# Kernel optimization log

Measured on AMD Instinct MI355X. Metric: run time of the kernel, lower is better.

## Reference

```python
import jax, jax.numpy as jnp
import numpy as np
from jax import lax


def _maxpool_nchw(x, k):
    # Non-overlapping kxk max pool over the last two dims (NCHW).
    return lax.reduce_window(x, -jnp.inf, lax.max,
                             window_dimensions=(1, 1, k, k),
                             window_strides=(1, 1, k, k),
                             padding='VALID')


def setup_inputs() -> dict:
    key = jax.random.key(0)
    k1, k2, k3, k4, k5 = jax.random.split(key, 5)
    B = 16
    return {
        'input_tensor1': jax.random.normal(k1, (B, 128, 48, 48), jnp.float32),
        'input_tensor2': jax.random.normal(k2, (B, 64, 96, 96), jnp.float32),
        'input_tensor3': jax.random.normal(k3, (B, 32, 192, 192), jnp.float32),
        'input_tensor4': jax.random.normal(k4, (B, 16, 384, 384), jnp.float32),
        'pure_ff': jax.random.normal(k5, (B, 256, 24, 24), jnp.float32),
    }


def reference(input_tensor1, input_tensor2, input_tensor3, input_tensor4, pure_ff):
    # and then max-pools. Pooling is per-channel, so this equals pooling once
    # and tiling the pooled result along the channel axis -- same math,
    # without materializing the redundant concat intermediates.
    x1 = jnp.tile(_maxpool_nchw(input_tensor1, 2), (1, 2, 1, 1))   # [B,256,24,24]
    x2 = jnp.tile(_maxpool_nchw(input_tensor2, 4), (1, 4, 1, 1))   # [B,256,24,24]
    x3 = jnp.tile(_maxpool_nchw(input_tensor3, 8), (1, 8, 1, 1))   # [B,256,24,24]
    x4 = jnp.tile(_maxpool_nchw(input_tensor4, 16), (1, 16, 1, 1)) # [B,256,24,24]
    return jax.nn.relu(x1 + x2 + x3 + x4 + pure_ff)
```

## Files before the change

### kernel.cpp

```cpp
#include <hip/hip_runtime.h>
#include <math.h>


namespace {

__device__ __forceinline__ float fmax4(const float4 v) {
  return fmaxf(fmaxf(v.x, v.y), fmaxf(v.z, v.w));
}
__device__ __forceinline__ float4 ld4(const float* p) {
  return *reinterpret_cast<const float4*>(p);
}

__global__ __launch_bounds__(256) void fused_block(const float* __restrict__ x1,
                                                   const float* __restrict__ x2,
                                                   const float* __restrict__ x3,
                                                   const float* __restrict__ x4,
                                                   const float* __restrict__ ff,
                                                   float* __restrict__ out) {
  __shared__ __attribute__((aligned(16))) float s1[128 * 6];
  __shared__ __attribute__((aligned(16))) float s2[64 * 6];
  __shared__ __attribute__((aligned(16))) float s3[32 * 6];
  __shared__ __attribute__((aligned(16))) float s4[16 * 6];

  const int blk = blockIdx.x;
  const int b   = blk / 96;
  const int rem = blk % 96;
  const int oh  = rem >> 2;
  const int q4  = rem & 3;
  const int tid = threadIdx.x;

#pragma unroll
  for (int it = 0; it < 6; ++it) {
    const int t = it * 256 + tid;
    if (t < 384) {
      const int ch = t / 3, pid = t % 3;
      const float* p = x1 + (size_t)(b * 128 + ch) * 2304 + oh * 2 * 48 + q4 * 12 + pid * 4;
      float4 v[2];
      v[0] = ld4(p);
      v[1] = ld4(p + 48);
      s1[ch * 6 + pid * 2]     = fmaxf(fmaxf(v[0].x, v[0].y), fmaxf(v[1].x, v[1].y));
      s1[ch * 6 + pid * 2 + 1] = fmaxf(fmaxf(v[0].z, v[0].w), fmaxf(v[1].z, v[1].w));
    } else if (t < 768) {
      const int u = t - 384;
      const int ch = u / 6, ow = u % 6;
      const float* p = x2 + (size_t)(b * 64 + ch) * 9216 + oh * 4 * 96 + (q4 * 6 + ow) * 4;
      float4 v[4];
#pragma unroll
      for (int r = 0; r < 4; ++r) v[r] = ld4(p + r * 96);
      float m = fmaxf(fmaxf(fmax4(v[0]), fmax4(v[1])), fmaxf(fmax4(v[2]), fmax4(v[3])));
      s2[ch * 6 + ow] = m;
    } else if (t < 1152) {
      const int u = t - 768;
      const int ch = u / 12, r2 = u % 12, ow = r2 >> 1, hf = r2 & 1;
      const float* p = x3 + (size_t)(b * 32 + ch) * 36864 + oh * 8 * 192 + (q4 * 6 + ow) * 8 + hf * 4;
      float4 v[8];
#pragma unroll
      for (int r = 0; r < 8; ++r) v[r] = ld4(p + r * 192);
      float m = -INFINITY;
#pragma unroll
      for (int r = 0; r < 8; ++r) m = fmaxf(m, fmax4(v[r]));
      m = fmaxf(m, __shfl_xor(m, 1));
      if (hf == 0) s3[ch * 6 + ow] = m;
    } else {
      const int u = t - 1152;
      const int ch = u / 24, r2 = u % 24, ow = r2 >> 2, qq = r2 & 3;
      const float* p = x4 + (size_t)(b * 16 + ch) * 147456 + oh * 16 * 384 + (q4 * 6 + ow) * 16 + qq * 4;
      float m = -INFINITY;
#pragma unroll
      for (int g = 0; g < 2; ++g) {
        float4 v[8];
#pragma unroll
        for (int r = 0; r < 8; ++r) v[r] = ld4(p + (g * 8 + r) * 384);
#pragma unroll
        for (int r = 0; r < 8; ++r) m = fmaxf(m, fmax4(v[r]));
      }
      m = fmaxf(m, __shfl_xor(m, 1));
      m = fmaxf(m, __shfl_xor(m, 2));
      if (qq == 0) s4[ch * 6 + ow] = m;
    }
  }

  __syncthreads();

#pragma unroll
  for (int it = 0; it < 3; ++it) {
    const int e = it * 256 + tid;
    const int c = e / 3, cp = e % 3;
    const float2 a1 = *reinterpret_cast<const float2*>(&s1[(c & 127) * 6 + cp * 2]);
    const float2 a2 = *reinterpret_cast<const float2*>(&s2[(c & 63)  * 6 + cp * 2]);
    const float2 a3 = *reinterpret_cast<const float2*>(&s3[(c & 31)  * 6 + cp * 2]);
    const float2 a4 = *reinterpret_cast<const float2*>(&s4[(c & 15)  * 6 + cp * 2]);
    const size_t o = (size_t)(b * 256 + c) * 576 + oh * 24 + q4 * 6 + cp * 2;
    const float2 f = *reinterpret_cast<const float2*>(ff + o);
    float2 r;
    r.x = fmaxf((((a1.x + a2.x) + a3.x) + a4.x) + f.x, 0.0f);
    r.y = fmaxf((((a1.y + a2.y) + a3.y) + a4.y) + f.y, 0.0f);
    *reinterpret_cast<float2*>(out + o) = r;
  }
}

}

extern "C" void kernel_launch(void* const* d_in, const int* in_sizes, int n_in,
                              void* d_out, int out_size, void* d_ws, size_t ws_size,
                              hipStream_t stream) {
  const float* x1 = (const float*)d_in[0];
  const float* x2 = (const float*)d_in[1];
  const float* x3 = (const float*)d_in[2];
  const float* x4 = (const float*)d_in[3];
  const float* ff = (const float*)d_in[4];
  float* out = (float*)d_out;
  (void)d_ws; (void)ws_size; (void)in_sizes; (void)n_in; (void)out_size;

  fused_block<<<1536, 256, 0, stream>>>(x1, x2, x3, x4, ff, out);
}
```

Measured before the change: 324.3 us.

## Use 384-thread blocks with each thread loading all four inputs upfront

The block grows from 256 to 384 threads so that every thread handles exactly one work item for each of the four pooled inputs, with no branching. All 30 float4 loads per thread are issued before any reduction, giving more memory-level parallelism and removing divergent branches within waves. The output loop drops from three iterations to two. Register pressure rises from holding 30 float4 values live at once, which may limit occupancy despite the launch_bounds(384,4) hint.

Result: no change. 328.8 us (+1.4%).

```diff
diff --git a/kernel.cpp b/kernel.cpp
--- a/kernel.cpp
+++ b/kernel.cpp
@@ -11,12 +11,12 @@
   return *reinterpret_cast<const float4*>(p);
 }
 
-__global__ __launch_bounds__(256) void fused_block(const float* __restrict__ x1,
-                                                   const float* __restrict__ x2,
-                                                   const float* __restrict__ x3,
-                                                   const float* __restrict__ x4,
-                                                   const float* __restrict__ ff,
-                                                   float* __restrict__ out) {
+__global__ __launch_bounds__(384, 4) void fused_block(const float* __restrict__ x1,
+                                                      const float* __restrict__ x2,
+                                                      const float* __restrict__ x3,
+                                                      const float* __restrict__ x4,
+                                                      const float* __restrict__ ff,
+                                                      float* __restrict__ out) {
   __shared__ __attribute__((aligned(16))) float s1[128 * 6];
   __shared__ __attribute__((aligned(16))) float s2[64 * 6];
   __shared__ __attribute__((aligned(16))) float s3[32 * 6];
@@ -29,63 +29,61 @@
   const int q4  = rem & 3;
   const int tid = threadIdx.x;
 
+  const int chA = tid / 3, pid = tid - chA * 3;
+  const float* pA = x1 + (size_t)(b * 128 + chA) * 2304 + oh * 96 + q4 * 12 + pid * 4;
+  const int chB = tid / 6, owB = tid - chB * 6;
+  const float* pB = x2 + (size_t)(b * 64 + chB) * 9216 + oh * 384 + (q4 * 6 + owB) * 4;
+  const int chC = tid / 12, rC = tid - chC * 12, owC = rC >> 1, hf = rC & 1;
+  const float* pC = x3 + (size_t)(b * 32 + chC) * 36864 + oh * 1536 + (q4 * 6 + owC) * 8 + hf * 4;
+  const int chD = tid / 24, rD = tid - chD * 24, owD = rD >> 2, qq = rD & 3;
+  const float* pD = x4 + (size_t)(b * 16 + chD) * 147456 + oh * 6144 + (q4 * 6 + owD) * 16 + qq * 4;
+
+  float4 va[2], vb[4], vc[8], vd[16];
 #pragma unroll
-  for (int it = 0; it < 6; ++it) {
-    const int t = it * 256 + tid;
-    if (t < 384) {
-      const int ch = t / 3, pid = t % 3;
-      const float* p = x1 + (size_t)(b * 128 + ch) * 2304 + oh * 2 * 48 + q4 * 12 + pid * 4;
-      float4 v[2];
-      v[0] = ld4(p);
-      v[1] = ld4(p + 48);
-      s1[ch * 6 + pid * 2]     = fmaxf(fmaxf(v[0].x, v[0].y), fmaxf(v[1].x, v[1].y));
-      s1[ch * 6 + pid * 2 + 1] = fmaxf(fmaxf(v[0].z, v[0].w), fmaxf(v[1].z, v[1].w));
-    } else if (t < 768) {
-      const int u = t - 384;
-      const int ch = u / 6, ow = u % 6;
-      const float* p = x2 + (size_t)(b * 64 + ch) * 9216 + oh * 4 * 96 + (q4 * 6 + ow) * 4;
-      float4 v[4];
+  for (int r = 0; r < 16; ++r) vd[r] = ld4(pD + r * 384);
 #pragma unroll
-      for (int r = 0; r < 4; ++r) v[r] = ld4(p + r * 96);
-      float m = fmaxf(fmaxf(fmax4(v[0]), fmax4(v[1])), fmaxf(fmax4(v[2]), fmax4(v[3])));
-      s2[ch * 6 + ow] = m;
-    } else if (t < 1152) {
-      const int u = t - 768;
-      const int ch = u / 12, r2 = u % 12, ow = r2 >> 1, hf = r2 & 1;
-      const float* p = x3 + (size_t)(b * 32 + ch) * 36864 + oh * 8 * 192 + (q4 * 6 + ow) * 8 + hf * 4;
-      float4 v[8];
+  for (int r = 0; r < 8; ++r) vc[r] = ld4(pC + r * 192);
 #pragma unroll
-      for (int r = 0; r < 8; ++r) v[r] = ld4(p + r * 192);
-      float m = -INFINITY;
+  for (int r = 0; r < 4; ++r) vb[r] = ld4(pB + r * 96);
 #pragma unroll
-      for (int r = 0; r < 8; ++r) m = fmaxf(m, fmax4(v[r]));
-      m = fmaxf(m, __shfl_xor(m, 1));
-      if (hf == 0) s3[ch * 6 + ow] = m;
-    } else {
-      const int u = t - 1152;
-      const int ch = u / 24, r2 = u % 24, ow = r2 >> 2, qq = r2 & 3;
-      const float* p = x4 + (size_t)(b * 16 + ch) * 147456 + oh * 16 * 384 + (q4 * 6 + ow) * 16 + qq * 4;
-      float m = -INFINITY;
-#pragma unroll
-      for (int g = 0; g < 2; ++g) {
-        float4 v[8];
-#pragma unroll
-        for (int r = 0; r < 8; ++r) v[r] = ld4(p + (g * 8 + r) * 384);
-#pragma unroll
-        for (int r = 0; r < 8; ++r) m = fmaxf(m, fmax4(v[r]));
-      }
-      m = fmaxf(m, __shfl_xor(m, 1));
-      m = fmaxf(m, __shfl_xor(m, 2));
-      if (qq == 0) s4[ch * 6 + ow] = m;
-    }
+  for (int r = 0; r < 2; ++r) va[r] = ld4(pA + r * 48);
+
+  {
+    float2 r2;
+    r2.x = fmaxf(fmaxf(va[0].x, va[0].y), fmaxf(va[1].x, va[1].y));
+    r2.y = fmaxf(fmaxf(va[0].z, va[0].w), fmaxf(va[1].z, va[1].w));
+    *reinterpret_cast<float2*>(&s1[chA * 6 + pid * 2]) = r2;
+  }
+  {
+    float m = fmaxf(fmaxf(fmax4(vb[0]), fmax4(vb[1])), fmaxf(fmax4(vb[2]), fmax4(vb[3])));
+    s2[chB * 6 + owB] = m;
+  }
+  {
+    float m0 = fmaxf(fmax4(vc[0]), fmax4(vc[1]));
+    float m1 = fmaxf(fmax4(vc[2]), fmax4(vc[3]));
+    float m2 = fmaxf(fmax4(vc[4]), fmax4(vc[5]));
+    float m3 = fmaxf(fmax4(vc[6]), fmax4(vc[7]));
+    float m  = fmaxf(fmaxf(m0, m1), fmaxf(m2, m3));
+    m = fmaxf(m, __shfl_xor(m, 1));
+    if (hf == 0) s3[chC * 6 + owC] = m;
+  }
+  {
+    float m0 = fmaxf(fmaxf(fmax4(vd[0]),  fmax4(vd[1])),  fmaxf(fmax4(vd[2]),  fmax4(vd[3])));
+    float m1 = fmaxf(fmaxf(fmax4(vd[4]),  fmax4(vd[5])),  fmaxf(fmax4(vd[6]),  fmax4(vd[7])));
+    float m2 = fmaxf(fmaxf(fmax4(vd[8]),  fmax4(vd[9])),  fmaxf(fmax4(vd[10]), fmax4(vd[11])));
+    float m3 = fmaxf(fmaxf(fmax4(vd[12]), fmax4(vd[13])), fmaxf(fmax4(vd[14]), fmax4(vd[15])));
+    float m  = fmaxf(fmaxf(m0, m1), fmaxf(m2, m3));
+    m = fmaxf(m, __shfl_xor(m, 1));
+    m = fmaxf(m, __shfl_xor(m, 2));
+    if (qq == 0) s4[chD * 6 + owD] = m;
   }
 
   __syncthreads();
 
 #pragma unroll
-  for (int it = 0; it < 3; ++it) {
-    const int e = it * 256 + tid;
-    const int c = e / 3, cp = e % 3;
+  for (int it = 0; it < 2; ++it) {
+    const int e = it * 384 + tid;
+    const int c = e / 3, cp = e - c * 3;
     const float2 a1 = *reinterpret_cast<const float2*>(&s1[(c & 127) * 6 + cp * 2]);
     const float2 a2 = *reinterpret_cast<const float2*>(&s2[(c & 63)  * 6 + cp * 2]);
     const float2 a3 = *reinterpret_cast<const float2*>(&s3[(c & 31)  * 6 + cp * 2]);
@@ -112,5 +110,5 @@
   float* out = (float*)d_out;
   (void)d_ws; (void)ws_size; (void)in_sizes; (void)n_in; (void)out_size;
 
-  fused_block<<<1536, 256, 0, stream>>>(x1, x2, x3, x4, ff, out);
+  fused_block<<<1536, 384, 0, stream>>>(x1, x2, x3, x4, ff, out);
 }
```
